# Optimization experiments

Measured on AMD Instinct MI355X. Metric: run time of the kernel, lower is better.

## Reference

```python
import jax, jax.numpy as jnp
import numpy as np

H, P = 16, 4  # n_heads, n_points


def setup_inputs() -> dict:
    B, L, D = 2, 4096, 1024
    rng = jax.random.key(0)
    ks = jax.random.split(rng, 12)
    w = lambda k, shape, s=0.02: jax.random.normal(k, shape, jnp.float32) * s
    return {
        "query": jax.random.normal(ks[0], (B, L, D), jnp.float32),
        "key": jax.random.normal(ks[1], (B, L, D), jnp.float32),
        "value": jax.random.normal(ks[2], (B, L, D), jnp.float32),
        "w_qk": w(ks[3], (D, 2 * D)), "b_qk": jnp.zeros((2 * D,), jnp.float32),
        "w_value": w(ks[4], (D, D)), "b_value": jnp.zeros((D,), jnp.float32),
        "w_off": w(ks[5], (D, H * P * 2)), "b_off": w(ks[6], (H * P * 2,), 0.3),
        "w_attw": w(ks[7], (D, H * P)), "b_attw": jnp.zeros((H * P,), jnp.float32),
        "w_out": w(ks[8], (D, D)), "b_out": jnp.zeros((D,), jnp.float32),
    }


def reference(query, key, value, w_qk, b_qk, w_value, b_value, w_off, b_off,
              w_attw, b_attw, w_out, b_out):
    B, L, D = value.shape
    Dh = D // H
    _qk = query @ w_qk + b_qk  # computed in torch forward but unused (dead code)
    # value projection -> (B, H, L, Dh)
    v = (value @ w_value + b_value).reshape(B, L, H, Dh).transpose(0, 2, 1, 3)
    off = (query @ w_off + b_off).reshape(B, L, H, P, 2)
    attw = jax.nn.softmax((query @ w_attw + b_attw).reshape(B, L, H, P), axis=-1)
    # effective reference point for query l (after the [:, :, :, :1, :] slice): (x=0, y=l/(L-1))
    ref_y = jnp.linspace(0.0, 1.0, L)
    sx = jnp.clip(off[..., 0], 0.0, 1.0)                                   # (B,L,H,P)
    sy = jnp.clip(ref_y[None, :, None, None] + off[..., 1], 0.0, 1.0)
    # F.grid_sample, align_corners=False, padding zeros, input shape (B*H, Dh, 1, L)
    ix = ((sx + 1.0) * L - 1.0) * 0.5
    iy = ((sy + 1.0) * 1.0 - 1.0) * 0.5
    x0 = jnp.floor(ix)
    fx = ix - x0
    x0i = x0.astype(jnp.int32)
    x1i = x0i + 1
    m0 = ((x0i >= 0) & (x0i < L)).astype(v.dtype)
    m1 = ((x1i >= 0) & (x1i < L)).astype(v.dtype)
    y0 = jnp.floor(iy)
    fy = iy - y0
    # height dim is 1: only row 0 valid, zero padding otherwise
    hy = jnp.where(y0 == 0.0, 1.0 - fy, 0.0) + jnp.where(y0 == -1.0, fy, 0.0)
    tr = lambda a: a.transpose(0, 2, 1, 3)  # (B,L,H,P) -> (B,H,L,P)

    def gather(idx):  # idx: (B,H,L,P) int32
        idxc = jnp.clip(idx, 0, L - 1).reshape(B, H, L * P, 1)
        return jnp.take_along_axis(v, idxc, axis=2).reshape(B, H, L, P, Dh)

    val0 = gather(tr(x0i))
    val1 = gather(tr(x1i))
    wx0 = tr((1.0 - fx) * m0 * hy)
    wx1 = tr(fx * m1 * hy)
    sampled = val0 * wx0[..., None] + val1 * wx1[..., None]  # (B,H,L,P,Dh)
    out = jnp.einsum('bhlpd,bhlp->blhd', sampled, tr(attw)).reshape(B, L, D)
    return out @ w_out + b_out
```

## Files before the change

kernel.cpp:

```cpp
#include <hip/hip_runtime.h>
#include <hip/hip_bf16.h>

typedef __bf16 bf16x8 __attribute__((ext_vector_type(8)));
typedef float f32x4 __attribute__((ext_vector_type(4)));

static __device__ __forceinline__ unsigned short f2bf(float x) {
    __hip_bfloat16 b = __float2bfloat16(x);
    return __builtin_bit_cast(unsigned short, b);
}
static __device__ __forceinline__ float bf2f(unsigned short u) {
    __hip_bfloat16 b = __builtin_bit_cast(__hip_bfloat16, u);
    return __bfloat162float(b);
}

static __device__ __forceinline__ void gload_lds16(const void* g, void* l) {
    __builtin_amdgcn_global_load_lds(
        (const __attribute__((address_space(1))) void*)g,
        (__attribute__((address_space(3))) void*)l, 16, 0, 0);
}

__global__ void prep_weights(const float* __restrict__ w_value, const float* __restrict__ w_out,
                             const float* __restrict__ w_off, const float* __restrict__ w_attw,
                             unsigned short* __restrict__ WvT, unsigned short* __restrict__ WoT,
                             unsigned short* __restrict__ WThi, unsigned short* __restrict__ WTlo) {
    __shared__ float tile[32][33];
    const int sel = blockIdx.y;
    const int k0 = blockIdx.x * 32;
    const int tx = threadIdx.x, ty = threadIdx.y;
    if (sel < 64) {
        const float* in = (sel < 32) ? w_value : w_out;
        unsigned short* out = (sel < 32) ? WvT : WoT;
        const int n0 = (sel & 31) * 32;
        for (int i = ty; i < 32; i += 8) tile[i][tx] = in[(size_t)(k0 + i) * 1024 + n0 + tx];
        __syncthreads();
        for (int i = ty; i < 32; i += 8)
            out[(size_t)(n0 + i) * 1024 + k0 + tx] = f2bf(tile[tx][i]);
    } else {
        const int n0 = (sel - 64) * 32;
        for (int i = ty; i < 32; i += 8) {
            int n = n0 + tx;
            tile[i][tx] = (n < 128) ? w_off[(size_t)(k0 + i) * 128 + n]
                                    : w_attw[(size_t)(k0 + i) * 64 + (n - 128)];
        }
        __syncthreads();
        for (int i = ty; i < 32; i += 8) {
            int n = n0 + i, k = k0 + tx;
            float v = tile[tx][i];
            unsigned short hi = f2bf(v);
            unsigned short lo = f2bf(v - bf2f(hi));
            WThi[(size_t)n * 1024 + k] = hi;
            WTlo[(size_t)n * 1024 + k] = lo;
        }
    }
}

__global__ __launch_bounds__(256, 2) void offw_mfma(
    const float* __restrict__ query,
    const unsigned short* __restrict__ WThi,
    const unsigned short* __restrict__ WTlo,
    float* __restrict__ part) {
    __shared__ unsigned short Ahi[64 * 32], Alo[64 * 32];
    __shared__ unsigned short Bs2[2 * 192 * 32];
    const int tid = threadIdx.x;
    const int lane = tid & 63, wave = tid >> 6;
    const int bm = blockIdx.x * 64;
    const int sk = blockIdx.y;
    const int r = lane & 15, kq = lane >> 4;

    f32x4 acc[4][3];
    #pragma unroll
    for (int i = 0; i < 4; ++i)
        #pragma unroll
        for (int j = 0; j < 3; ++j) acc[i][j] = (f32x4){0.f, 0.f, 0.f, 0.f};

    const int arow = tid >> 2;
    const int apos = (tid & 3) * 8;

    for (int k0 = sk * 256; k0 < sk * 256 + 256; k0 += 32) {
        const float* qp = query + (size_t)(bm + arow) * 1024 + k0 + apos;
        float4 qa = reinterpret_cast<const float4*>(qp)[0];
        float4 qb = reinterpret_cast<const float4*>(qp)[1];
        unsigned int hw[4], lw[4];
        {
            float4 qf[2] = {qa, qb};
            #pragma unroll
            for (int t = 0; t < 2; ++t) {
                float e0 = qf[t].x, e1 = qf[t].y, e2 = qf[t].z, e3 = qf[t].w;
                unsigned short h0 = f2bf(e0), h1 = f2bf(e1), h2 = f2bf(e2), h3 = f2bf(e3);
                unsigned short l0 = f2bf(e0 - bf2f(h0)), l1 = f2bf(e1 - bf2f(h1));
                unsigned short l2 = f2bf(e2 - bf2f(h2)), l3 = f2bf(e3 - bf2f(h3));
                hw[t * 2] = (unsigned int)h0 | ((unsigned int)h1 << 16);
                hw[t * 2 + 1] = (unsigned int)h2 | ((unsigned int)h3 << 16);
                lw[t * 2] = (unsigned int)l0 | ((unsigned int)l1 << 16);
                lw[t * 2 + 1] = (unsigned int)l2 | ((unsigned int)l3 << 16);
            }
        }
        *reinterpret_cast<uint4*>(&Ahi[arow * 32 + apos]) = (uint4){hw[0], hw[1], hw[2], hw[3]};
        *reinterpret_cast<uint4*>(&Alo[arow * 32 + apos]) = (uint4){lw[0], lw[1], lw[2], lw[3]};
        #pragma unroll
        for (int t = 0; t < 6; ++t) {
            int c = tid + 256 * t;
            int plane = (c >= 768);
            int cp = c - 768 * plane;
            const unsigned short* src = (plane ? WTlo : WThi)
                + (size_t)(cp >> 2) * 1024 + k0 + (cp & 3) * 8;
            gload_lds16(src, &Bs2[(size_t)(c & ~63) * 8]);
        }
        __syncthreads();

        bf16x8 bh[3], bl[3];
        #pragma unroll
        for (int j = 0; j < 3; ++j) {
            int ro = (wave * 48 + j * 16 + r) * 32 + kq * 8;
            bh[j] = *reinterpret_cast<const bf16x8*>(&Bs2[ro]);
            bl[j] = *reinterpret_cast<const bf16x8*>(&Bs2[192 * 32 + ro]);
        }
        #pragma unroll
        for (int i = 0; i < 4; ++i) {
            int ro = (i * 16 + r) * 32 + kq * 8;
            bf16x8 ah = *reinterpret_cast<const bf16x8*>(&Ahi[ro]);
            bf16x8 al = *reinterpret_cast<const bf16x8*>(&Alo[ro]);
            #pragma unroll
            for (int j = 0; j < 3; ++j) {
                acc[i][j] = __builtin_amdgcn_mfma_f32_16x16x32_bf16(ah, bh[j], acc[i][j], 0, 0, 0);
                acc[i][j] = __builtin_amdgcn_mfma_f32_16x16x32_bf16(ah, bl[j], acc[i][j], 0, 0, 0);
                acc[i][j] = __builtin_amdgcn_mfma_f32_16x16x32_bf16(al, bh[j], acc[i][j], 0, 0, 0);
            }
        }
        __syncthreads();
    }

    float* P = part + (size_t)sk * 8192 * 192;
    #pragma unroll
    for (int i = 0; i < 4; ++i) {
        int row0 = bm + i * 16 + kq * 4;
        #pragma unroll
        for (int j = 0; j < 3; ++j) {
            int col = wave * 48 + j * 16 + r;
            #pragma unroll
            for (int rr = 0; rr < 4; ++rr)
                P[(size_t)(row0 + rr) * 192 + col] = acc[i][j][rr];
        }
    }
}

__global__ __launch_bounds__(256, 2) void vproj_mfma(
    const float* __restrict__ value,
    const unsigned short* __restrict__ WvT,
    const float* __restrict__ bias,
    unsigned short* __restrict__ Vproj) {
    __shared__ unsigned short As[64 * 32];
    __shared__ unsigned short Bs[128 * 32];
    const int tid = threadIdx.x;
    const int lane = tid & 63, wave = tid >> 6;
    const int bm = 1920 + blockIdx.z * 4096 + blockIdx.x * 64;
    const int bn = blockIdx.y * 128;
    const int wr = wave >> 1, wc = wave & 1;
    const int r = lane & 15, kq = lane >> 4;

    f32x4 acc[2][4];
    #pragma unroll
    for (int i = 0; i < 2; ++i)
        #pragma unroll
        for (int j = 0; j < 4; ++j) acc[i][j] = (f32x4){0.f, 0.f, 0.f, 0.f};

    const int arow = tid >> 2;
    const int apos = (tid & 3) * 8;

    for (int k0 = 0; k0 < 1024; k0 += 32) {
        const float* vp = value + (size_t)(bm + arow) * 1024 + k0 + apos;
        float4 qa = reinterpret_cast<const float4*>(vp)[0];
        float4 qb = reinterpret_cast<const float4*>(vp)[1];
        unsigned int hw[4];
        hw[0] = (unsigned int)f2bf(qa.x) | ((unsigned int)f2bf(qa.y) << 16);
        hw[1] = (unsigned int)f2bf(qa.z) | ((unsigned int)f2bf(qa.w) << 16);
        hw[2] = (unsigned int)f2bf(qb.x) | ((unsigned int)f2bf(qb.y) << 16);
        hw[3] = (unsigned int)f2bf(qb.z) | ((unsigned int)f2bf(qb.w) << 16);
        *reinterpret_cast<uint4*>(&As[arow * 32 + apos]) = (uint4){hw[0], hw[1], hw[2], hw[3]};
        #pragma unroll
        for (int t = 0; t < 2; ++t) {
            int c = tid + 256 * t;
            gload_lds16(WvT + (size_t)(bn + (c >> 2)) * 1024 + k0 + (c & 3) * 8,
                        &Bs[(size_t)(c & ~63) * 8]);
        }
        __syncthreads();

        bf16x8 af[2], bfr[4];
        #pragma unroll
        for (int i = 0; i < 2; ++i)
            af[i] = *reinterpret_cast<const bf16x8*>(&As[(wr * 32 + i * 16 + r) * 32 + kq * 8]);
        #pragma unroll
        for (int j = 0; j < 4; ++j)
            bfr[j] = *reinterpret_cast<const bf16x8*>(&Bs[(wc * 64 + j * 16 + r) * 32 + kq * 8]);
        #pragma unroll
        for (int i = 0; i < 2; ++i)
            #pragma unroll
            for (int j = 0; j < 4; ++j)
                acc[i][j] = __builtin_amdgcn_mfma_f32_16x16x32_bf16(af[i], bfr[j], acc[i][j], 0, 0, 0);
        __syncthreads();
    }

    #pragma unroll
    for (int i = 0; i < 2; ++i) {
        int row0 = bm + wr * 32 + i * 16 + kq * 4;
        #pragma unroll
        for (int j = 0; j < 4; ++j) {
            int col = bn + wc * 64 + j * 16 + r;
            float bs = bias[col];
            #pragma unroll
            for (int rr = 0; rr < 4; ++rr)
                Vproj[(size_t)(row0 + rr) * 1024 + col] = f2bf(acc[i][j][rr] + bs);
        }
    }
}

__global__ __launch_bounds__(256) void sample_coef(
    const float* __restrict__ part, const float* __restrict__ b_off,
    const float* __restrict__ b_attw, const unsigned short* __restrict__ vproj,
    unsigned short* __restrict__ s_out) {
    const int n = blockIdx.x;
    const int tid = threadIdx.x;
    const int l = n & 4095;
    __shared__ float Ls[192];
    __shared__ int sIdx[64];
    __shared__ float sC0[64], sC1[64];
    if (tid < 192) {
        const size_t SK = (size_t)8192 * 192;
        const float* Pn = part + (size_t)n * 192 + tid;
        float s = (tid < 128) ? b_off[tid] : b_attw[tid - 128];
        Ls[tid] = s + Pn[0] + Pn[SK] + Pn[2 * SK] + Pn[3 * SK];
    }
    __syncthreads();
    if (tid < 64) {
        int h = tid >> 2, p = tid & 3;
        float l0 = Ls[128 + h * 4 + 0], l1 = Ls[128 + h * 4 + 1];
        float l2 = Ls[128 + h * 4 + 2], l3 = Ls[128 + h * 4 + 3];
        float mx = fmaxf(fmaxf(l0, l1), fmaxf(l2, l3));
        float e0 = expf(l0 - mx), e1 = expf(l1 - mx), e2 = expf(l2 - mx), e3 = expf(l3 - mx);
        float esum = e0 + e1 + e2 + e3;
        float aw = ((p == 0) ? e0 : (p == 1) ? e1 : (p == 2) ? e2 : e3) / esum;
        float o0 = Ls[h * 8 + p * 2], o1 = Ls[h * 8 + p * 2 + 1];
        float sx = fminf(fmaxf(o0, 0.f), 1.f);
        float ry = (float)l / 4095.0f;
        float sy = fminf(fmaxf(ry + o1, 0.f), 1.f);
        float ix = ((sx + 1.f) * 4096.f - 1.f) * 0.5f;
        float iy = sy * 0.5f;
        float x0f = floorf(ix);
        float fx = ix - x0f;
        int x0 = (int)x0f;
        int x1 = x0 + 1;
        float m0 = (x0 >= 0 && x0 < 4096) ? 1.f : 0.f;
        float m1 = (x1 >= 0 && x1 < 4096) ? 1.f : 0.f;
        float y0f = floorf(iy);
        float fy = iy - y0f;
        float hy = ((y0f == 0.f) ? (1.f - fy) : 0.f) + ((y0f == -1.f) ? fy : 0.f);
        sC0[tid] = aw * (1.f - fx) * m0 * hy;
        sC1[tid] = aw * fx * m1 * hy;
        sIdx[tid] = x0 < 0 ? 0 : (x0 > 4095 ? 4095 : x0);
    }
    __syncthreads();
    const int d = tid * 4;
    const int h = tid >> 4;
    const size_t vb = (size_t)(n >> 12) * 4096 * 1024;
    float a0 = 0.f, a1 = 0.f, a2 = 0.f, a3 = 0.f;
    #pragma unroll
    for (int p = 0; p < 4; ++p) {
        int e = h * 4 + p;
        int x0 = sIdx[e];
        float c0 = sC0[e], c1 = sC1[e];
        int x1 = (x0 + 1 > 4095) ? 4095 : x0 + 1;
        ushort4 v0 = *reinterpret_cast<const ushort4*>(vproj + vb + (size_t)x0 * 1024 + d);
        ushort4 v1 = *reinterpret_cast<const ushort4*>(vproj + vb + (size_t)x1 * 1024 + d);
        a0 += c0 * bf2f(v0.x) + c1 * bf2f(v1.x);
        a1 += c0 * bf2f(v0.y) + c1 * bf2f(v1.y);
        a2 += c0 * bf2f(v0.z) + c1 * bf2f(v1.z);
        a3 += c0 * bf2f(v0.w) + c1 * bf2f(v1.w);
    }
    ushort4 o;
    o.x = f2bf(a0); o.y = f2bf(a1); o.z = f2bf(a2); o.w = f2bf(a3);
    *reinterpret_cast<ushort4*>(s_out + (size_t)n * 1024 + d) = o;
}

__global__ __launch_bounds__(256, 2) void gemm_bt(
    const unsigned short* __restrict__ A,
    const unsigned short* __restrict__ Bt,
    const float* __restrict__ bias,
    float* __restrict__ C, int N, int K) {
    __shared__ unsigned short As[128 * 32];
    __shared__ unsigned short Bs[128 * 32];
    const int tid = threadIdx.x;
    const int lane = tid & 63;
    const int wave = tid >> 6;
    const int bm = blockIdx.x * 128;
    const int bn = blockIdx.y * 128;
    const int wr = wave >> 1;
    const int wc = wave & 1;
    const int r = lane & 15;
    const int kq = lane >> 4;

    f32x4 acc[4][4];
    #pragma unroll
    for (int i = 0; i < 4; ++i)
        #pragma unroll
        for (int j = 0; j < 4; ++j) acc[i][j] = (f32x4){0.f, 0.f, 0.f, 0.f};

    const int c1 = tid;
    const int c2 = 256 + tid;
    const int cb1 = wave * 64;
    const int cb2 = 256 + wave * 64;

    for (int k0 = 0; k0 < K; k0 += 32) {
        const unsigned short* Ab = A + (size_t)bm * K + k0;
        const unsigned short* Bb = Bt + (size_t)bn * K + k0;
        gload_lds16(Ab + (size_t)(c1 >> 2) * K + (c1 & 3) * 8, &As[cb1 * 8]);
        gload_lds16(Ab + (size_t)(c2 >> 2) * K + (c2 & 3) * 8, &As[cb2 * 8]);
        gload_lds16(Bb + (size_t)(c1 >> 2) * K + (c1 & 3) * 8, &Bs[cb1 * 8]);
        gload_lds16(Bb + (size_t)(c2 >> 2) * K + (c2 & 3) * 8, &Bs[cb2 * 8]);
        __syncthreads();

        bf16x8 af[4], bfr[4];
        #pragma unroll
        for (int i = 0; i < 4; ++i)
            af[i] = *reinterpret_cast<const bf16x8*>(&As[(wr * 64 + i * 16 + r) * 32 + kq * 8]);
        #pragma unroll
        for (int j = 0; j < 4; ++j)
            bfr[j] = *reinterpret_cast<const bf16x8*>(&Bs[(wc * 64 + j * 16 + r) * 32 + kq * 8]);
        #pragma unroll
        for (int i = 0; i < 4; ++i)
            #pragma unroll
            for (int j = 0; j < 4; ++j)
                acc[i][j] = __builtin_amdgcn_mfma_f32_16x16x32_bf16(af[i], bfr[j], acc[i][j], 0, 0, 0);
        __syncthreads();
    }

    #pragma unroll
    for (int i = 0; i < 4; ++i) {
        int row0 = bm + wr * 64 + i * 16 + kq * 4;
        #pragma unroll
        for (int j = 0; j < 4; ++j) {
            int col = bn + wc * 64 + j * 16 + r;
            float bs = bias[col];
            #pragma unroll
            for (int rr = 0; rr < 4; ++rr)
                C[(size_t)(row0 + rr) * N + col] = acc[i][j][rr] + bs;
        }
    }
}

extern "C" void kernel_launch(void* const* d_in, const int* in_sizes, int n_in,
                              void* d_out, int out_size, void* d_ws, size_t ws_size,
                              hipStream_t stream) {
    const float* query  = (const float*)d_in[0];
    const float* value  = (const float*)d_in[2];
    const float* w_value = (const float*)d_in[5];
    const float* b_value = (const float*)d_in[6];
    const float* w_off   = (const float*)d_in[7];
    const float* b_off   = (const float*)d_in[8];
    const float* w_attw  = (const float*)d_in[9];
    const float* b_attw  = (const float*)d_in[10];
    const float* w_out   = (const float*)d_in[11];
    const float* b_out   = (const float*)d_in[12];
    float* out = (float*)d_out;

    char* w = (char*)d_ws;
    unsigned short* WvT   = (unsigned short*)(w + (16ull << 20));
    unsigned short* WoT   = (unsigned short*)(w + (18ull << 20));
    unsigned short* Vproj = (unsigned short*)(w + (20ull << 20));
    unsigned short* S     = (unsigned short*)(w + (36ull << 20));
    unsigned short* WThi  = (unsigned short*)(w + (53ull << 20));
    unsigned short* WTlo  = (unsigned short*)(w + (54ull << 20));
    float*          Part  = (float*)(w + (56ull << 20));

    prep_weights<<<dim3(32, 70), dim3(32, 8), 0, stream>>>(
        w_value, w_out, w_off, w_attw, WvT, WoT, WThi, WTlo);
    offw_mfma<<<dim3(128, 4), 256, 0, stream>>>(query, WThi, WTlo, Part);
    vproj_mfma<<<dim3(34, 8, 2), 256, 0, stream>>>(value, WvT, b_value, Vproj);
    sample_coef<<<8192, 256, 0, stream>>>(Part, b_off, b_attw, Vproj, S);
    gemm_bt<<<dim3(64, 8), 256, 0, stream>>>(S, WoT, b_out, out, 1024, 1024);
}
```

Measured before the change: 99.80 us.

## Pre-convert value rows to bf16 and load both GEMM operands via direct LDS loads

A new combined prep kernel converts the needed value rows (L>=1920) from fp32 to bf16 in workspace, alongside the existing weight transposes. The value-projection GEMM then loads A tiles with global_load_lds instead of fp32 loads plus in-register conversion. Its tiling is also reshaped to 128x64, with each wave taking 32 rows. This trades an extra write and read of a bf16 copy of value for a leaner, asynchronous GEMM inner loop, and the B tile is now reused across more rows.

Result: faster. 94.28 us (-5.5%).

```diff
diff --git a/kernel.cpp b/kernel.cpp
--- a/kernel.cpp
+++ b/kernel.cpp
@@ -19,14 +19,32 @@
         (__attribute__((address_space(3))) void*)l, 16, 0, 0);
 }
 
-__global__ void prep_weights(const float* __restrict__ w_value, const float* __restrict__ w_out,
-                             const float* __restrict__ w_off, const float* __restrict__ w_attw,
-                             unsigned short* __restrict__ WvT, unsigned short* __restrict__ WoT,
-                             unsigned short* __restrict__ WThi, unsigned short* __restrict__ WTlo) {
+__global__ __launch_bounds__(256) void prep_all(
+    const float* __restrict__ w_value, const float* __restrict__ w_out,
+    const float* __restrict__ w_off, const float* __restrict__ w_attw,
+    const float* __restrict__ value,
+    unsigned short* __restrict__ WvT, unsigned short* __restrict__ WoT,
+    unsigned short* __restrict__ WThi, unsigned short* __restrict__ WTlo,
+    unsigned short* __restrict__ Vbf) {
+    const int bid = blockIdx.x;
+    const int tid = threadIdx.x;
+    if (bid >= 2240) {
+        int g = (bid - 2240) * 256 + tid;
+        int r4 = g >> 8;
+        int cpos = g & 255;
+        int b = r4 / 2176;
+        int l = 1920 + (r4 % 2176);
+        size_t off4 = (size_t)(b * 4096 + l) * 256 + cpos;
+        float4 v = reinterpret_cast<const float4*>(value)[off4];
+        ushort4 o;
+        o.x = f2bf(v.x); o.y = f2bf(v.y); o.z = f2bf(v.z); o.w = f2bf(v.w);
+        reinterpret_cast<ushort4*>(Vbf)[off4] = o;
+        return;
+    }
     __shared__ float tile[32][33];
-    const int sel = blockIdx.y;
-    const int k0 = blockIdx.x * 32;
-    const int tx = threadIdx.x, ty = threadIdx.y;
+    const int sel = bid >> 5;
+    const int k0 = (bid & 31) * 32;
+    const int tx = tid & 31, ty = tid >> 5;
     if (sel < 64) {
         const float* in = (sel < 32) ? w_value : w_out;
         unsigned short* out = (sel < 32) ? WvT : WoT;
@@ -145,17 +163,16 @@
 }
 
 __global__ __launch_bounds__(256, 2) void vproj_mfma(
-    const float* __restrict__ value,
+    const unsigned short* __restrict__ Vbf,
     const unsigned short* __restrict__ WvT,
     const float* __restrict__ bias,
     unsigned short* __restrict__ Vproj) {
-    __shared__ unsigned short As[64 * 32];
-    __shared__ unsigned short Bs[128 * 32];
+    __shared__ unsigned short As[128 * 32];
+    __shared__ unsigned short Bs[64 * 32];
     const int tid = threadIdx.x;
     const int lane = tid & 63, wave = tid >> 6;
-    const int bm = 1920 + blockIdx.z * 4096 + blockIdx.x * 64;
-    const int bn = blockIdx.y * 128;
-    const int wr = wave >> 1, wc = wave & 1;
+    const int bm = 1920 + blockIdx.z * 4096 + blockIdx.x * 128;
+    const int bn = blockIdx.y * 64;
     const int r = lane & 15, kq = lane >> 4;
 
     f32x4 acc[2][4];
@@ -164,34 +181,25 @@
         #pragma unroll
         for (int j = 0; j < 4; ++j) acc[i][j] = (f32x4){0.f, 0.f, 0.f, 0.f};
 
-    const int arow = tid >> 2;
-    const int apos = (tid & 3) * 8;
+    const int c1 = tid;
+    const int c2 = 256 + tid;
 
     for (int k0 = 0; k0 < 1024; k0 += 32) {
-        const float* vp = value + (size_t)(bm + arow) * 1024 + k0 + apos;
-        float4 qa = reinterpret_cast<const float4*>(vp)[0];
-        float4 qb = reinterpret_cast<const float4*>(vp)[1];
-        unsigned int hw[4];
-        hw[0] = (unsigned int)f2bf(qa.x) | ((unsigned int)f2bf(qa.y) << 16);
-        hw[1] = (unsigned int)f2bf(qa.z) | ((unsigned int)f2bf(qa.w) << 16);
-        hw[2] = (unsigned int)f2bf(qb.x) | ((unsigned int)f2bf(qb.y) << 16);
-        hw[3] = (unsigned int)f2bf(qb.z) | ((unsigned int)f2bf(qb.w) << 16);
-        *reinterpret_cast<uint4*>(&As[arow * 32 + apos]) = (uint4){hw[0], hw[1], hw[2], hw[3]};
-        #pragma unroll
-        for (int t = 0; t < 2; ++t) {
-            int c = tid + 256 * t;
-            gload_lds16(WvT + (size_t)(bn + (c >> 2)) * 1024 + k0 + (c & 3) * 8,
-                        &Bs[(size_t)(c & ~63) * 8]);
-        }
+        gload_lds16(Vbf + (size_t)(bm + (c1 >> 2)) * 1024 + k0 + (c1 & 3) * 8,
+                    &As[(size_t)(c1 & ~63) * 8]);
+        gload_lds16(Vbf + (size_t)(bm + (c2 >> 2)) * 1024 + k0 + (c2 & 3) * 8,
+                    &As[(size_t)(256 + (tid & ~63)) * 8]);
+        gload_lds16(WvT + (size_t)(bn + (tid >> 2)) * 1024 + k0 + (tid & 3) * 8,
+                    &Bs[(size_t)(tid & ~63) * 8]);
         __syncthreads();
 
         bf16x8 af[2], bfr[4];
         #pragma unroll
         for (int i = 0; i < 2; ++i)
-            af[i] = *reinterpret_cast<const bf16x8*>(&As[(wr * 32 + i * 16 + r) * 32 + kq * 8]);
+            af[i] = *reinterpret_cast<const bf16x8*>(&As[(wave * 32 + i * 16 + r) * 32 + kq * 8]);
         #pragma unroll
         for (int j = 0; j < 4; ++j)
-            bfr[j] = *reinterpret_cast<const bf16x8*>(&Bs[(wc * 64 + j * 16 + r) * 32 + kq * 8]);
+            bfr[j] = *reinterpret_cast<const bf16x8*>(&Bs[(j * 16 + r) * 32 + kq * 8]);
         #pragma unroll
         for (int i = 0; i < 2; ++i)
             #pragma unroll
@@ -202,10 +210,10 @@
 
     #pragma unroll
     for (int i = 0; i < 2; ++i) {
-        int row0 = bm + wr * 32 + i * 16 + kq * 4;
+        int row0 = bm + wave * 32 + i * 16 + kq * 4;
         #pragma unroll
         for (int j = 0; j < 4; ++j) {
-            int col = bn + wc * 64 + j * 16 + r;
+            int col = bn + j * 16 + r;
             float bs = bias[col];
             #pragma unroll
             for (int rr = 0; rr < 4; ++rr)
@@ -363,6 +371,7 @@
     float* out = (float*)d_out;
 
     char* w = (char*)d_ws;
+    unsigned short* Vbf   = (unsigned short*)(w);
     unsigned short* WvT   = (unsigned short*)(w + (16ull << 20));
     unsigned short* WoT   = (unsigned short*)(w + (18ull << 20));
     unsigned short* Vproj = (unsigned short*)(w + (20ull << 20));
@@ -371,10 +380,10 @@
     unsigned short* WTlo  = (unsigned short*)(w + (54ull << 20));
     float*          Part  = (float*)(w + (56ull << 20));
 
-    prep_weights<<<dim3(32, 70), dim3(32, 8), 0, stream>>>(
-        w_value, w_out, w_off, w_attw, WvT, WoT, WThi, WTlo);
+    prep_all<<<6592, 256, 0, stream>>>(w_value, w_out, w_off, w_attw, value,
+                                       WvT, WoT, WThi, WTlo, Vbf);
     offw_mfma<<<dim3(128, 4), 256, 0, stream>>>(query, WThi, WTlo, Part);
-    vproj_mfma<<<dim3(34, 8, 2), 256, 0, stream>>>(value, WvT, b_value, Vproj);
+    vproj_mfma<<<dim3(17, 16, 2), 256, 0, stream>>>(Vbf, WvT, b_value, Vproj);
     sample_coef<<<8192, 256, 0, stream>>>(Part, b_off, b_attw, Vproj, S);
     gemm_bt<<<dim3(64, 8), 256, 0, stream>>>(S, WoT, b_out, out, 1024, 1024);
 }
```
